# Optimization experiments

Hardware: AMD Instinct MI355X
Metric: run time of the kernel (lower is better)

Reference implementation:

```python
import jax, jax.numpy as jnp
import numpy as np

B, N, D, H = 8, 2048, 256, 4
HD = D // H


def setup_inputs() -> dict:
    key = jax.random.key(0)
    ks = jax.random.split(key, 12)
    s = 1.0 / np.sqrt(D)
    inp = {
        "node_features": jax.random.normal(ks[0], (B, N, D), dtype=jnp.float32),
        "causal_mask": jnp.tril(jnp.ones((N, N), dtype=jnp.float32)),
        "Wq": jax.random.normal(ks[1], (D, D), dtype=jnp.float32) * s,
        "bq": jnp.zeros((D,), dtype=jnp.float32),
        "Wk": jax.random.normal(ks[2], (D, D), dtype=jnp.float32) * s,
        "bk": jnp.zeros((D,), dtype=jnp.float32),
        "Wv": jax.random.normal(ks[3], (D, D), dtype=jnp.float32) * s,
        "bv": jnp.zeros((D,), dtype=jnp.float32),
        "Wo": jax.random.normal(ks[4], (D, D), dtype=jnp.float32) * s,
        "bo": jnp.zeros((D,), dtype=jnp.float32),
        "Wu": jax.random.normal(ks[5], (2 * D, D), dtype=jnp.float32) * (1.0 / np.sqrt(2 * D)),
        "bu": jnp.zeros((D,), dtype=jnp.float32),
    }
    return inp


def reference(node_features, causal_mask, Wq, bq, Wk, bk, Wv, bv, Wo, bo, Wu, bu):
    # node_features: [B, N, D]; causal_mask: [N, N] (1 = keep, 0 = masked)
    x = node_features
    # project and split heads -> [B, H, N, HD]
    def heads(w, b):
        return (x @ w + b).reshape(B, N, H, HD).transpose(0, 2, 1, 3)
    q, k, v = heads(Wq, bq), heads(Wk, bk), heads(Wv, bv)
    scale = 1.0 / np.sqrt(HD).astype(np.float32)
    scores = jnp.einsum("bhnd,bhmd->bhnm", q, k) * scale  # [B, H, N, N]
    scores = jnp.where(causal_mask > 0, scores, jnp.float32(-1e9))
    attn = jax.nn.softmax(scores, axis=-1)
    ctx = jnp.einsum("bhnm,bhmd->bhnd", attn, v)  # [B, H, N, HD]
    messages = ctx.transpose(0, 2, 1, 3).reshape(B, N, D) @ Wo + bo  # [B, N, D]
    combined = jnp.concatenate([x, messages], axis=-1)  # [B, N, 2D]
    updated = jax.nn.relu(combined @ Wu + bu)  # [B, N, D]  (dropout = identity in eval)
    return updated
```

## Files before the change

kernel.cpp:

```cpp
#include <hip/hip_runtime.h>
#include <math.h>

constexpr int B  = 8;
constexpr int N  = 2048;
constexpr int D  = 256;
constexpr int H  = 4;
constexpr int HD = 64;
constexpr int MTOT = B * N;

typedef __attribute__((ext_vector_type(8))) short  short8;
typedef __attribute__((ext_vector_type(4))) float  floatx4;
typedef unsigned short ushort_t;

#define QSCALE 0.1803368801111204f

__device__ __forceinline__ unsigned short f2bf(float f) {
    unsigned u = __float_as_uint(f);
    u += 0x7fffu + ((u >> 16) & 1u);
    return (unsigned short)(u >> 16);
}

__global__ __launch_bounds__(256) void cvt_x(
    const float* __restrict__ x, ushort_t* __restrict__ xb)
{
    int idx = (blockIdx.x * 256 + threadIdx.x) * 8;
    float4 a = *(const float4*)(x + idx);
    float4 b = *(const float4*)(x + idx + 4);
    ushort_t o[8] = {f2bf(a.x), f2bf(a.y), f2bf(a.z), f2bf(a.w),
                     f2bf(b.x), f2bf(b.y), f2bf(b.z), f2bf(b.w)};
    *(short8*)(xb + idx) = *(const short8*)o;
}

__global__ __launch_bounds__(256) void cvt_wt(
    const float* __restrict__ Wq, const float* __restrict__ Wk,
    const float* __restrict__ Wv, const float* __restrict__ Wo,
    const float* __restrict__ Wu,
    ushort_t* __restrict__ wqkvt, ushort_t* __restrict__ wot,
    ushort_t* __restrict__ wut)
{
    __shared__ float Ls[64][65];
    const int z = blockIdx.z;
    const float* src; ushort_t* dst; int K;
    if      (z == 0) { src = Wq; dst = wqkvt;          K = 256; }
    else if (z == 1) { src = Wk; dst = wqkvt + 65536;  K = 256; }
    else if (z == 2) { src = Wv; dst = wqkvt + 131072; K = 256; }
    else if (z == 3) { src = Wo; dst = wot;            K = 256; }
    else             { src = Wu; dst = wut;            K = 512; }
    const int kt = blockIdx.y, nt = blockIdx.x;
    if (kt * 64 >= K) return;
    const int t = threadIdx.x;
    #pragma unroll
    for (int i = 0; i < 16; i++) {
        int e = t + i * 256, r = e >> 6, c = e & 63;
        Ls[r][c] = src[(size_t)(kt * 64 + r) * 256 + nt * 64 + c];
    }
    __syncthreads();
    #pragma unroll
    for (int i = 0; i < 16; i++) {
        int e = t + i * 256, r = e >> 6, c = e & 63;
        dst[(size_t)(nt * 64 + r) * K + kt * 64 + c] = f2bf(Ls[c][r]);
    }
}

__global__ __launch_bounds__(256) void qkv_gemm(
    const ushort_t* __restrict__ xb, const ushort_t* __restrict__ wqkvt,
    const float* __restrict__ bq, const float* __restrict__ bk,
    const float* __restrict__ bv,
    ushort_t* __restrict__ q, ushort_t* __restrict__ kout,
    ushort_t* __restrict__ vt)
{
    __shared__ ushort_t SH[17408];
    ushort_t* As = SH;
    ushort_t* Bs = SH + 8704;

    const int t = threadIdx.x, w = t >> 6, lane = t & 63;
    const int quad = lane >> 4, l16 = lane & 15;
    const int bx = blockIdx.x;
    const int col0 = bx * 128, row0 = blockIdx.y * 128;
    const int wr = (w >> 1) * 64, wc = (w & 1) * 64;

    floatx4 acc[4][4] = {};

    for (int k0 = 0; k0 < 256; k0 += 64) {
        __syncthreads();
        #pragma unroll
        for (int i = 0; i < 4; i++) {
            int e = t + (i << 8);
            int r = e >> 3, c8 = (e & 7) << 3;
            *(short8*)&As[r * 68 + c8] =
                *(const short8*)(xb + (size_t)(row0 + r) * 256 + k0 + c8);
            *(short8*)&Bs[r * 68 + c8] =
                *(const short8*)(wqkvt + (size_t)(col0 + r) * 256 + k0 + c8);
        }
        __syncthreads();

        #pragma unroll
        for (int kk = 0; kk < 64; kk += 32) {
            short8 af[4], bf[4];
            #pragma unroll
            for (int i = 0; i < 4; i++)
                af[i] = *(const short8*)&As[(wr + i * 16 + l16) * 68 + kk + quad * 8];
            #pragma unroll
            for (int j = 0; j < 4; j++)
                bf[j] = *(const short8*)&Bs[(wc + j * 16 + l16) * 68 + kk + quad * 8];
            #pragma unroll
            for (int i = 0; i < 4; i++)
                #pragma unroll
                for (int j = 0; j < 4; j++)
                    acc[i][j] = __builtin_amdgcn_mfma_f32_16x16x32_bf16(
                        af[i], bf[j], acc[i][j], 0, 0, 0);
        }
    }

    const int kind = bx >> 1;
    const float* bias = (kind == 0) ? bq : (kind == 1 ? bk : bv);
    const float scl  = (kind == 0) ? QSCALE : 1.0f;
    __syncthreads();
    ushort_t (*Ts)[132] = (ushort_t(*)[132])SH;
    #pragma unroll
    for (int j = 0; j < 4; j++) {
        int cl = wc + j * 16 + l16;
        float bsv = bias[(bx & 1) * 128 + cl];
        #pragma unroll
        for (int i = 0; i < 4; i++) {
            #pragma unroll
            for (int r = 0; r < 4; r++) {
                int ml = wr + i * 16 + quad * 4 + r;
                ushort_t bvv = f2bf((acc[i][j][r] + bsv) * scl);
                if (kind < 2) Ts[ml][cl] = bvv;
                else          Ts[cl][ml] = bvv;
            }
        }
    }
    __syncthreads();

    const int b = row0 >> 11, n0 = row0 & (N - 1);
    #pragma unroll
    for (int i = 0; i < 8; i++) {
        int id = t + (i << 8);
        int rr = id >> 4, c8 = (id & 15) << 3;
        short8 val = *(const short8*)&Ts[rr][c8];
        if (kind < 2) {
            int cg = (bx & 1) * 128 + c8;
            int h = cg >> 6, hd = cg & 63;
            ushort_t* dst = (kind == 0) ? q : kout;
            *(short8*)&dst[(((size_t)(b * H + h)) * N + n0 + rr) * HD + hd] = val;
        } else {
            int cg = (bx & 1) * 128 + rr;
            int h = cg >> 6, hd = cg & 63;
            *(short8*)&vt[(((size_t)(b * H + h)) * HD + hd) * N + n0 + c8] = val;
        }
    }
}

__global__ __launch_bounds__(256) void attn_mfma(
    const ushort_t* __restrict__ q,
    const ushort_t* __restrict__ k,
    const ushort_t* __restrict__ vt,
    ushort_t* __restrict__ ctxb)
{
    __shared__ ushort_t Ks [128][68];
    __shared__ ushort_t Vts[64][132];
    __shared__ ushort_t Ps [4][16][132];

    const int t    = threadIdx.x;
    const int w    = t >> 6;
    const int lane = t & 63;
    const int quad = lane >> 4;
    const int l16  = lane & 15;
    const int bh   = blockIdx.x;
    const int b    = bh >> 2, h = bh & 3;

    const ushort_t* qp = q  + (size_t)bh * N * HD;
    const ushort_t* kp = k  + (size_t)bh * N * HD;
    const ushort_t* vp = vt + (size_t)bh * HD * N;

    for (int pass = 0; pass < 2; pass++) {
        const int qt    = (pass == 0) ? (31 - (int)blockIdx.y) : (int)blockIdx.y;
        const int qbase = qt * 64;
        const int rowb  = qbase + w * 16;

        short8 qf0, qf1;
        {
            const ushort_t* qrow = qp + (size_t)(rowb + l16) * HD + quad * 8;
            qf0 = *(const short8*)(qrow);
            qf1 = *(const short8*)(qrow + 32);
        }

        floatx4 acc_o[4] = {};
        float plsum[4] = {};

        const int nkt = (qt >> 1) + 1;
        for (int kt = 0; kt < nkt; kt++) {
            const int kbase = kt * 128;
            __syncthreads();

            #pragma unroll
            for (int i = 0; i < 4; i++) {
                int e  = t + (i << 8);
                int kr = e >> 3, kc = (e & 7) << 3;
                *(short8*)&Ks[kr][kc] =
                    *(const short8*)(kp + (size_t)(kbase + kr) * HD + kc);
                int vr = e >> 4, vc = (e & 15) << 3;
                *(short8*)&Vts[vr][vc] =
                    *(const short8*)(vp + (size_t)vr * N + kbase + vc);
            }
            __syncthreads();

            int rem = rowb + 15 - kbase;
            int nch = (rem < 0) ? 0 : ((rem >> 5) + 1);
            if (nch > 4) nch = 4;

            for (int ch = 0; ch < nch; ch++) {
                #pragma unroll
                for (int c2 = 0; c2 < 2; c2++) {
                    const int ct = ch * 2 + c2;
                    short8 kf0 = *(const short8*)&Ks[ct * 16 + l16][quad * 8];
                    short8 kf1 = *(const short8*)&Ks[ct * 16 + l16][32 + quad * 8];
                    floatx4 z = {0.0f, 0.0f, 0.0f, 0.0f};
                    floatx4 s = __builtin_amdgcn_mfma_f32_16x16x32_bf16(qf0, kf0, z, 0, 0, 0);
                    s         = __builtin_amdgcn_mfma_f32_16x16x32_bf16(qf1, kf1, s, 0, 0, 0);
                    const bool partial = (kbase + ct * 16 + 15) > rowb;
                    const int  keyg    = kbase + ct * 16 + l16;
                    #pragma unroll
                    for (int r = 0; r < 4; r++) {
                        float sv = s[r];
                        if (partial && keyg > rowb + quad * 4 + r) sv = -3.0e38f;
                        float pv = __builtin_amdgcn_exp2f(sv);
                        plsum[r] += pv;
                        Ps[w][quad * 4 + r][ct * 16 + l16] = f2bf(pv);
                    }
                }
                short8 pf = *(const short8*)&Ps[w][l16][ch * 32 + quad * 8];
                #pragma unroll
                for (int nt = 0; nt < 4; nt++) {
                    short8 vf = *(const short8*)&Vts[nt * 16 + l16][ch * 32 + quad * 8];
                    acc_o[nt] = __builtin_amdgcn_mfma_f32_16x16x32_bf16(pf, vf, acc_o[nt], 0, 0, 0);
                }
            }
        }

        #pragma unroll
        for (int r = 0; r < 4; r++) {
            float l = plsum[r];
            l += __shfl_xor(l, 1);
            l += __shfl_xor(l, 2);
            l += __shfl_xor(l, 4);
            l += __shfl_xor(l, 8);
            float inv = 1.0f / l;
            int   n   = rowb + quad * 4 + r;
            #pragma unroll
            for (int nt = 0; nt < 4; nt++) {
                ctxb[((size_t)(b * N + n)) * D + h * HD + nt * 16 + l16] =
                    f2bf(acc_o[nt][r] * inv);
            }
        }
    }
}

__global__ __launch_bounds__(256) void tail_k(
    const ushort_t* __restrict__ ctxb, const ushort_t* __restrict__ xb,
    const ushort_t* __restrict__ wot,  const ushort_t* __restrict__ wut,
    const float* __restrict__ bo, const float* __restrict__ bu,
    float* __restrict__ out)
{
    __shared__ ushort_t As1[32][68];
    __shared__ ushort_t Bs [256][68];
    __shared__ ushort_t msgS[32][260];

    const int t = threadIdx.x, w = t >> 6, lane = t & 63;
    const int quad = lane >> 4, l16 = lane & 15;
    const int row0 = blockIdx.x * 32;
    const int wc = w * 64;

    floatx4 acc1[2][4] = {};
    for (int k0 = 0; k0 < 256; k0 += 64) {
        __syncthreads();
        {
            int rr = t >> 3, c8 = (t & 7) << 3;
            *(short8*)&As1[rr][c8] =
                *(const short8*)(ctxb + (size_t)(row0 + rr) * 256 + k0 + c8);
        }
        #pragma unroll
        for (int i = 0; i < 8; i++) {
            int e = t + (i << 8);
            int nr = e >> 3, c8 = (e & 7) << 3;
            *(short8*)&Bs[nr][c8] =
                *(const short8*)(wot + (size_t)nr * 256 + k0 + c8);
        }
        __syncthreads();

        #pragma unroll
        for (int kk = 0; kk < 64; kk += 32) {
            short8 af[2], bf[4];
            #pragma unroll
            for (int i = 0; i < 2; i++)
                af[i] = *(const short8*)&As1[i * 16 + l16][kk + quad * 8];
            #pragma unroll
            for (int j = 0; j < 4; j++)
                bf[j] = *(const short8*)&Bs[wc + j * 16 + l16][kk + quad * 8];
            #pragma unroll
            for (int i = 0; i < 2; i++)
                #pragma unroll
                for (int j = 0; j < 4; j++)
                    acc1[i][j] = __builtin_amdgcn_mfma_f32_16x16x32_bf16(
                        af[i], bf[j], acc1[i][j], 0, 0, 0);
        }
    }
    #pragma unroll
    for (int j = 0; j < 4; j++) {
        int col = wc + j * 16 + l16;
        float bsv = bo[col];
        #pragma unroll
        for (int i = 0; i < 2; i++)
            #pragma unroll
            for (int r = 0; r < 4; r++)
                msgS[i * 16 + quad * 4 + r][col] = f2bf(acc1[i][j][r] + bsv);
    }

    floatx4 acc2[2][4] = {};
    for (int k0 = 0; k0 < 512; k0 += 64) {
        const bool xpart = (k0 < 256);
        __syncthreads();
        if (xpart) {
            int rr = t >> 3, c8 = (t & 7) << 3;
            *(short8*)&As1[rr][c8] =
                *(const short8*)(xb + (size_t)(row0 + rr) * 256 + k0 + c8);
        }
        #pragma unroll
        for (int i = 0; i < 8; i++) {
            int e = t + (i << 8);
            int nr = e >> 3, c8 = (e & 7) << 3;
            *(short8*)&Bs[nr][c8] =
                *(const short8*)(wut + (size_t)nr * 512 + k0 + c8);
        }
        __syncthreads();

        #pragma unroll
        for (int kk = 0; kk < 64; kk += 32) {
            short8 af[2], bf[4];
            #pragma unroll
            for (int i = 0; i < 2; i++) {
                if (xpart)
                    af[i] = *(const short8*)&As1[i * 16 + l16][kk + quad * 8];
                else
                    af[i] = *(const short8*)&msgS[i * 16 + l16][(k0 - 256) + kk + quad * 8];
            }
            #pragma unroll
            for (int j = 0; j < 4; j++)
                bf[j] = *(const short8*)&Bs[wc + j * 16 + l16][kk + quad * 8];
            #pragma unroll
            for (int i = 0; i < 2; i++)
                #pragma unroll
                for (int j = 0; j < 4; j++)
                    acc2[i][j] = __builtin_amdgcn_mfma_f32_16x16x32_bf16(
                        af[i], bf[j], acc2[i][j], 0, 0, 0);
        }
    }

    #pragma unroll
    for (int j = 0; j < 4; j++) {
        int col = wc + j * 16 + l16;
        float bsv = bu[col];
        #pragma unroll
        for (int i = 0; i < 2; i++) {
            #pragma unroll
            for (int r = 0; r < 4; r++) {
                int m = row0 + i * 16 + quad * 4 + r;
                out[(size_t)m * 256 + col] = fmaxf(acc2[i][j][r] + bsv, 0.0f);
            }
        }
    }
}

extern "C" void kernel_launch(void* const* d_in, const int* in_sizes, int n_in,
                              void* d_out, int out_size, void* d_ws, size_t ws_size,
                              hipStream_t stream)
{
    const float* x  = (const float*)d_in[0];
    const float* Wq = (const float*)d_in[2];
    const float* bq = (const float*)d_in[3];
    const float* Wk = (const float*)d_in[4];
    const float* bk = (const float*)d_in[5];
    const float* Wv = (const float*)d_in[6];
    const float* bv = (const float*)d_in[7];
    const float* Wo = (const float*)d_in[8];
    const float* bo = (const float*)d_in[9];
    const float* Wu = (const float*)d_in[10];
    const float* bu = (const float*)d_in[11];
    float* out = (float*)d_out;

    const size_t SZ = (size_t)MTOT * D;
    ushort_t* xb    = (ushort_t*)d_ws;
    ushort_t* qb    = xb    + SZ;
    ushort_t* kb    = qb    + SZ;
    ushort_t* vbt   = kb    + SZ;
    ushort_t* ctxb  = vbt   + SZ;
    ushort_t* wqkvt = ctxb  + SZ;
    ushort_t* wot   = wqkvt + 196608;
    ushort_t* wut   = wot   + 65536;

    cvt_x<<<2048, 256, 0, stream>>>(x, xb);
    cvt_wt<<<dim3(4, 8, 5), 256, 0, stream>>>(Wq, Wk, Wv, Wo, Wu,
                                              wqkvt, wot, wut);

    qkv_gemm<<<dim3(6, 128), 256, 0, stream>>>(xb, wqkvt, bq, bk, bv,
                                               qb, kb, vbt);

    attn_mfma<<<dim3(32, 16), 256, 0, stream>>>(qb, kb, vbt, ctxb);

    tail_k<<<512, 256, 0, stream>>>(ctxb, xb, wot, wut, bo, bu, out);
}
```

Baseline: 205.1 us.

## Process 128-row query tiles per block, sharing K/V loads across strips

The attention kernel no longer runs two balanced passes over 64-row query tiles. Each block now handles one 128-row query tile, and each wave computes two 16-row strips against the same shared K/V tile. This roughly halves global-to-LDS K/V traffic and barrier rounds, and the two independent strips give more MFMA ILP. The cost is that the old pairing of long and short causal tiles is gone, so per-block work is now uneven (heavy tiles are scheduled first). Register use also rises from the doubled accumulators.

```diff
diff --git a/kernel.cpp b/kernel.cpp
--- a/kernel.cpp
+++ b/kernel.cpp
@@ -161,7 +161,7 @@
 {
     __shared__ ushort_t Ks [128][68];
     __shared__ ushort_t Vts[64][132];
-    __shared__ ushort_t Ps [4][16][132];
+    __shared__ ushort_t Ps [4][2][16][36];
 
     const int t    = threadIdx.x;
     const int w    = t >> 6;
@@ -170,89 +170,117 @@
     const int l16  = lane & 15;
     const int bh   = blockIdx.x;
     const int b    = bh >> 2, h = bh & 3;
+    const int qt2  = 15 - (int)blockIdx.y;
+    const int qbase = qt2 * 128;
 
     const ushort_t* qp = q  + (size_t)bh * N * HD;
     const ushort_t* kp = k  + (size_t)bh * N * HD;
     const ushort_t* vp = vt + (size_t)bh * HD * N;
 
-    for (int pass = 0; pass < 2; pass++) {
-        const int qt    = (pass == 0) ? (31 - (int)blockIdx.y) : (int)blockIdx.y;
-        const int qbase = qt * 64;
-        const int rowb  = qbase + w * 16;
-
-        short8 qf0, qf1;
-        {
-            const ushort_t* qrow = qp + (size_t)(rowb + l16) * HD + quad * 8;
-            qf0 = *(const short8*)(qrow);
-            qf1 = *(const short8*)(qrow + 32);
-        }
-
-        floatx4 acc_o[4] = {};
-        float plsum[4] = {};
-
-        const int nkt = (qt >> 1) + 1;
-        for (int kt = 0; kt < nkt; kt++) {
-            const int kbase = kt * 128;
-            __syncthreads();
-
-            #pragma unroll
-            for (int i = 0; i < 4; i++) {
-                int e  = t + (i << 8);
-                int kr = e >> 3, kc = (e & 7) << 3;
-                *(short8*)&Ks[kr][kc] =
-                    *(const short8*)(kp + (size_t)(kbase + kr) * HD + kc);
-                int vr = e >> 4, vc = (e & 15) << 3;
-                *(short8*)&Vts[vr][vc] =
-                    *(const short8*)(vp + (size_t)vr * N + kbase + vc);
-            }
-            __syncthreads();
-
-            int rem = rowb + 15 - kbase;
-            int nch = (rem < 0) ? 0 : ((rem >> 5) + 1);
-            if (nch > 4) nch = 4;
-
-            for (int ch = 0; ch < nch; ch++) {
-                #pragma unroll
-                for (int c2 = 0; c2 < 2; c2++) {
-                    const int ct = ch * 2 + c2;
-                    short8 kf0 = *(const short8*)&Ks[ct * 16 + l16][quad * 8];
-                    short8 kf1 = *(const short8*)&Ks[ct * 16 + l16][32 + quad * 8];
-                    floatx4 z = {0.0f, 0.0f, 0.0f, 0.0f};
-                    floatx4 s = __builtin_amdgcn_mfma_f32_16x16x32_bf16(qf0, kf0, z, 0, 0, 0);
-                    s         = __builtin_amdgcn_mfma_f32_16x16x32_bf16(qf1, kf1, s, 0, 0, 0);
-                    const bool partial = (kbase + ct * 16 + 15) > rowb;
-                    const int  keyg    = kbase + ct * 16 + l16;
+    const int rowb[2] = { qbase + w * 16, qbase + 64 + w * 16 };
+
+    short8 qf[2][2];
+    #pragma unroll
+    for (int s = 0; s < 2; s++) {
+        const ushort_t* qrow = qp + (size_t)(rowb[s] + l16) * HD + quad * 8;
+        qf[s][0] = *(const short8*)(qrow);
+        qf[s][1] = *(const short8*)(qrow + 32);
+    }
+
+    floatx4 acc_o[2][4] = {};
+    float plsum[2][4] = {};
+
+    const int nkt = qt2 + 1;
+    for (int kt = 0; kt < nkt; kt++) {
+        const int kbase = kt * 128;
+        __syncthreads();
+
+        #pragma unroll
+        for (int i = 0; i < 4; i++) {
+            int e  = t + (i << 8);
+            int kr = e >> 3, kc = (e & 7) << 3;
+            *(short8*)&Ks[kr][kc] =
+                *(const short8*)(kp + (size_t)(kbase + kr) * HD + kc);
+            int vr = e >> 4, vc = (e & 15) << 3;
+            *(short8*)&Vts[vr][vc] =
+                *(const short8*)(vp + (size_t)vr * N + kbase + vc);
+        }
+        __syncthreads();
+
+        int nch[2];
+        #pragma unroll
+        for (int s = 0; s < 2; s++) {
+            int rem = rowb[s] + 15 - kbase;
+            int nc  = (rem < 0) ? 0 : ((rem >> 5) + 1);
+            nch[s] = (nc > 4) ? 4 : nc;
+        }
+
+        for (int ch = 0; ch < nch[1]; ch++) {
+            floatx4 sreg[2][2];
+            #pragma unroll
+            for (int s = 0; s < 2; s++) {
+                if (ch < nch[s]) {
                     #pragma unroll
-                    for (int r = 0; r < 4; r++) {
-                        float sv = s[r];
-                        if (partial && keyg > rowb + quad * 4 + r) sv = -3.0e38f;
-                        float pv = __builtin_amdgcn_exp2f(sv);
-                        plsum[r] += pv;
-                        Ps[w][quad * 4 + r][ct * 16 + l16] = f2bf(pv);
+                    for (int c2 = 0; c2 < 2; c2++) {
+                        const int ct = ch * 2 + c2;
+                        short8 kf0 = *(const short8*)&Ks[ct * 16 + l16][quad * 8];
+                        short8 kf1 = *(const short8*)&Ks[ct * 16 + l16][32 + quad * 8];
+                        floatx4 z = {0.0f, 0.0f, 0.0f, 0.0f};
+                        floatx4 sv = __builtin_amdgcn_mfma_f32_16x16x32_bf16(qf[s][0], kf0, z, 0, 0, 0);
+                        sv         = __builtin_amdgcn_mfma_f32_16x16x32_bf16(qf[s][1], kf1, sv, 0, 0, 0);
+                        sreg[s][c2] = sv;
                     }
                 }
-                short8 pf = *(const short8*)&Ps[w][l16][ch * 32 + quad * 8];
-                #pragma unroll
-                for (int nt = 0; nt < 4; nt++) {
-                    short8 vf = *(const short8*)&Vts[nt * 16 + l16][ch * 32 + quad * 8];
-                    acc_o[nt] = __builtin_amdgcn_mfma_f32_16x16x32_bf16(pf, vf, acc_o[nt], 0, 0, 0);
+            }
+            #pragma unroll
+            for (int s = 0; s < 2; s++) {
+                if (ch < nch[s]) {
+                    #pragma unroll
+                    for (int c2 = 0; c2 < 2; c2++) {
+                        const int keyb    = kbase + ch * 32 + c2 * 16;
+                        const bool partial = (keyb + 15) > rowb[s];
+                        const int  keyg    = keyb + l16;
+                        #pragma unroll
+                        for (int r = 0; r < 4; r++) {
+                            float sv = sreg[s][c2][r];
+                            if (partial && keyg > rowb[s] + quad * 4 + r) sv = -3.0e38f;
+                            float pv = __builtin_amdgcn_exp2f(sv);
+                            plsum[s][r] += pv;
+                            Ps[w][s][quad * 4 + r][c2 * 16 + l16] = f2bf(pv);
+                        }
+                    }
                 }
             }
-        }
-
+            #pragma unroll
+            for (int s = 0; s < 2; s++) {
+                if (ch < nch[s]) {
+                    short8 pf = *(const short8*)&Ps[w][s][l16][quad * 8];
+                    #pragma unroll
+                    for (int nt = 0; nt < 4; nt++) {
+                        short8 vf = *(const short8*)&Vts[nt * 16 + l16][ch * 32 + quad * 8];
+                        acc_o[s][nt] = __builtin_amdgcn_mfma_f32_16x16x32_bf16(
+                            pf, vf, acc_o[s][nt], 0, 0, 0);
+                    }
+                }
+            }
+        }
+    }
+
+    #pragma unroll
+    for (int s = 0; s < 2; s++) {
         #pragma unroll
         for (int r = 0; r < 4; r++) {
-            float l = plsum[r];
+            float l = plsum[s][r];
             l += __shfl_xor(l, 1);
             l += __shfl_xor(l, 2);
             l += __shfl_xor(l, 4);
             l += __shfl_xor(l, 8);
             float inv = 1.0f / l;
-            int   n   = rowb + quad * 4 + r;
+            int   n   = rowb[s] + quad * 4 + r;
             #pragma unroll
             for (int nt = 0; nt < 4; nt++) {
                 ctxb[((size_t)(b * N + n)) * D + h * HD + nt * 16 + l16] =
-                    f2bf(acc_o[nt][r] * inv);
+                    f2bf(acc_o[s][nt][r] * inv);
             }
         }
     }
```

New measurement: 216.6 us. +5.6%, slower.
